# Kernel optimization log

Hardware: AMD Instinct MI355X
Metric: run time of the kernel (lower is better)

## Reference

```python
import jax, jax.numpy as jnp
import numpy as np

NTOKENS = 8192
TOPK = 2
E = 8
K = 1024  # hidden
N = 1024  # ffn shard (ffn_hidden // ffn_tp)


def setup_inputs() -> dict:
    key = jax.random.key(0)
    k1, k2, k3 = jax.random.split(key, 3)
    x = jax.random.normal(k1, (NTOKENS, K), jnp.float32) * 0.02
    # weights stored [E, N, K] (transpose_weight=True path in the torch module)
    weights = jax.random.normal(k2, (E, N, K), jnp.float32) * 0.02
    # random top-k expert assignment per token, then derive the expert-sorted
    # dispatch permutation (scatter_index) and per-expert counts (splits),
    # exactly the invariants flux.prepare_moe_ag_scatter_args relies on.
    experts = jax.random.randint(k3, (NTOKENS, TOPK), 0, E)
    flat = experts.reshape(-1)                       # [NTOKENS*TOPK]
    order = jnp.argsort(flat, stable=True)           # output row -> flat slot
    m = NTOKENS * TOPK
    pos = jnp.zeros((m,), jnp.int32).at[order].set(jnp.arange(m, dtype=jnp.int32))
    scatter_index = pos.reshape(NTOKENS, TOPK)       # flat slot -> output row
    splits = jnp.bincount(flat, length=E).astype(jnp.int32)
    return {"x": x, "weights": weights, "scatter_index": scatter_index, "splits": splits}


def reference(x, weights, scatter_index, splits):
    """MoE AG-scatter grouped GEMM (single-rank semantics: all-gather = identity).

    For each output row s (rows sorted by expert): out[s] = x[token(s)] @ W[e(s)].T
    where token(s) = gather_A_index[s] // topk and e(s) comes from splits.
    """
    ntokens, topk = scatter_index.shape
    e, n, k = weights.shape
    m_out = ntokens * topk  # total dispatched rows
    # inverse permutation: output row s -> flattened (token, slot) index
    gather_a = jnp.argsort(scatter_index.reshape(-1), stable=True)  # [m_out]
    token_of_row = gather_a // topk                                  # [m_out]
    expert_of_row = jnp.repeat(jnp.arange(e, dtype=jnp.int32), splits,
                               total_repeat_length=m_out)            # [m_out]
    # compute each token against every expert once (E/topk redundancy), then
    # gather the (token, expert) pairs -- avoids per-row weight materialization
    y_all = jnp.einsum('tk,enk->ten', x, weights)   # [ntokens, E, N]
    out = y_all[token_of_row, expert_of_row]        # [m_out, N]
    return out
```

## Files before the change

### kernel.cpp

```cpp
#include <hip/hip_runtime.h>
#include <hip/hip_bf16.h>

#define NTOK   8192
#define TOPK   2
#define NEXP   8
#define KDIM   1024
#define NDIM   1024
#define MOUT   (NTOK * TOPK)
#define BM     128
#define BN     128
#define BK     64
#define MAXT   (MOUT / BM + NEXP)
#define NBLK   (MAXT * (NDIM / BN))
#define CLSCAP (NBLK / 8)

#define ROWTOK   16384
#define XB_OFF   (128 * 1024)
#define XB_BYTES (NTOK * KDIM * 2)
#define WB_OFF   (XB_OFF + XB_BYTES)
#define WB_BYTES (NEXP * NDIM * KDIM * 2)
#define WS_NEED  ((size_t)(WB_OFF + WB_BYTES))

typedef unsigned short ushort_t;
typedef __attribute__((ext_vector_type(8))) short short8;
typedef __attribute__((ext_vector_type(4))) float floatx4;
typedef __attribute__((address_space(1))) const unsigned int gu32;
typedef __attribute__((address_space(3))) unsigned int lu32;

__device__ __forceinline__ void map_block(int b, const int* __restrict__ splits,
                                          int& row0, int& rows, int& e_out,
                                          int& cy) {
  int sp[8], off[8], n[8], take[8];
  int o = 0;
#pragma unroll
  for (int e = 0; e < 8; ++e) {
    sp[e] = splits[e];
    off[e] = o;
    o += sp[e];
    int tiles = (sp[e] + BM - 1) / BM;
    n[e] = 8 * tiles;
    take[e] = (n[e] < CLSCAP) ? n[e] : CLSCAP;
  }
  const int c = b & 7, i = b >> 3;
  int e = -1, j = 0;
  if (i < take[c]) {
    e = c; j = i;
  } else {
    int freeBefore = 0;
#pragma unroll
    for (int cc = 0; cc < 8; ++cc)
      if (cc < c) freeBefore += CLSCAP - take[cc];
    int spos = freeBefore + (i - take[c]);
    int acc = 0;
#pragma unroll
    for (int ee = 0; ee < 8; ++ee) {
      int sp_e = n[ee] - take[ee];
      if (e < 0 && spos < acc + sp_e) { e = ee; j = CLSCAP + (spos - acc); }
      acc += sp_e;
    }
    if (e < 0) { rows = 0; return; }
  }
  int t = j >> 3;
  cy = j & 7;
  row0 = off[e] + t * BM;
  int rem = off[e] + sp[e] - row0;
  rows = (rem > BM) ? BM : rem;
  if (rows < 0) rows = 0;
  e_out = e;
}

__global__ __launch_bounds__(256)
void convert_setup(const float* __restrict__ x, const float* __restrict__ w,
                   const int* __restrict__ scatter,
                   ushort_t* __restrict__ xb, ushort_t* __restrict__ wb,
                   int* __restrict__ ws) {
  const int N4X = NTOK * KDIM / 4;
  const int N4W = NEXP * NDIM * KDIM / 4;
  int gtid = blockIdx.x * 256 + threadIdx.x;

  if (gtid < MOUT) {
    int s = scatter[gtid];
    ws[ROWTOK + s] = gtid / TOPK;
  }

  for (int i = gtid; i < N4X + N4W; i += gridDim.x * 256) {
    float4 v = (i < N4X) ? ((const float4*)x)[i] : ((const float4*)w)[i - N4X];
    union { __hip_bfloat162 h; unsigned int u; } lo, hi;
    lo.h = __float22bfloat162_rn(make_float2(v.x, v.y));
    hi.h = __float22bfloat162_rn(make_float2(v.z, v.w));
    uint2 u2; u2.x = lo.u; u2.y = hi.u;
    if (i < N4X) ((uint2*)xb)[i] = u2;
    else         ((uint2*)wb)[i - N4X] = u2;
  }
}

__global__ __launch_bounds__(256, 3)
void moe_gemm_fast(const ushort_t* __restrict__ xb,
                   const ushort_t* __restrict__ wbm,
                   const int* __restrict__ splits,
                   const int* __restrict__ ws,
                   float* __restrict__ out) {
  __shared__ ushort_t As[BM * BK];
  __shared__ ushort_t Bs[BN * BK];

  int row0, rows, e, cyi;
  map_block(blockIdx.x, splits, row0, rows, e, cyi);
  if (rows == 0) return;
  const int c0 = cyi * BN;

  const int tid  = threadIdx.x;
  const int lane = tid & 63;
  const int wave = tid >> 6;
  const int wm   = (wave >> 1) * 64;
  const int wn   = (wave & 1) * 64;
  const int quad = lane >> 4;
  const int l16  = lane & 15;

  const int* __restrict__ row_token = ws + ROWTOK;

  const int lrow8  = lane >> 3;
  const int gchunk = (lane & 7) ^ lrow8;

  const ushort_t* aptr[4];
  const ushort_t* bptr[4];
#pragma unroll
  for (int t = 0; t < 4; ++t) {
    int r  = wave * 32 + t * 8 + lrow8;
    int rc = (r < rows) ? r : (rows - 1);
    aptr[t] = xb + (size_t)row_token[row0 + rc] * KDIM + gchunk * 8;
    bptr[t] = wbm + ((size_t)e * NDIM + c0 + r) * KDIM + gchunk * 8;
  }

  floatx4 zero = {0.f, 0.f, 0.f, 0.f};
  floatx4 acc[4][4];
#pragma unroll
  for (int i = 0; i < 4; ++i)
#pragma unroll
    for (int j = 0; j < 4; ++j) acc[i][j] = zero;

#pragma unroll 4
  for (int kk = 0; kk < KDIM; kk += BK) {
#pragma unroll
    for (int t = 0; t < 4; ++t) {
      __builtin_amdgcn_global_load_lds(
          (gu32*)(const void*)(aptr[t] + kk),
          (lu32*)(void*)(As + (wave * 32 + t * 8) * BK), 16, 0, 0);
      __builtin_amdgcn_global_load_lds(
          (gu32*)(const void*)(bptr[t] + kk),
          (lu32*)(void*)(Bs + (wave * 32 + t * 8) * BK), 16, 0, 0);
    }
    __syncthreads();

#pragma unroll
    for (int k2 = 0; k2 < 2; ++k2) {
      short8 af[4], bf[4];
#pragma unroll
      for (int i = 0; i < 4; ++i) {
        int m = wm + i * 16 + l16;
        af[i] = *(const short8*)(&As[m * BK + (((k2 * 4 + quad) ^ (m & 7)) * 8)]);
      }
#pragma unroll
      for (int j = 0; j < 4; ++j) {
        int n = wn + j * 16 + l16;
        bf[j] = *(const short8*)(&Bs[n * BK + (((k2 * 4 + quad) ^ (n & 7)) * 8)]);
      }
#pragma unroll
      for (int i = 0; i < 4; ++i)
#pragma unroll
        for (int j = 0; j < 4; ++j)
          acc[i][j] = __builtin_amdgcn_mfma_f32_16x16x32_bf16(af[i], bf[j],
                                                              acc[i][j], 0, 0, 0);
    }
    __syncthreads();
  }

#pragma unroll
  for (int i = 0; i < 4; ++i) {
#pragma unroll
    for (int r = 0; r < 4; ++r) {
      int lrow = wm + i * 16 + quad * 4 + r;
      if (lrow < rows) {
        float* o = out + (size_t)(row0 + lrow) * NDIM + c0 + wn + l16;
#pragma unroll
        for (int j = 0; j < 4; ++j) o[j * 16] = acc[i][j][r];
      }
    }
  }
}

__global__ void setup_only(const int* __restrict__ scatter,
                           int* __restrict__ ws) {
  int gtid = blockIdx.x * blockDim.x + threadIdx.x;
  if (gtid < MOUT) {
    int s = scatter[gtid];
    ws[ROWTOK + s] = gtid / TOPK;
  }
}

__global__ __launch_bounds__(256)
void moe_gemm_fallback(const float* __restrict__ x,
                       const float* __restrict__ w,
                       const int* __restrict__ splits,
                       const int* __restrict__ ws,
                       float* __restrict__ out) {
  __shared__ ushort_t As[BM * BK];
  __shared__ ushort_t Bs[BN * BK];

  int row0, rows, e, cyi;
  map_block(blockIdx.x, splits, row0, rows, e, cyi);
  if (rows == 0) return;
  const int c0 = cyi * BN;

  const int tid  = threadIdx.x;
  const int lane = tid & 63;
  const int wave = tid >> 6;
  const int wm   = (wave >> 1) * 64;
  const int wn   = (wave & 1) * 64;
  const int quad = lane >> 4;
  const int l16  = lane & 15;

  const int* __restrict__ row_token = ws + ROWTOK;

  const int f4    = tid & 15;
  const int rbase = tid >> 4;
  const int swz   = (f4 >> 1) ^ (rbase & 7);
  const int wroff = rbase * BK + swz * 8 + (f4 & 1) * 4;

  const float* __restrict__ wb = w + ((size_t)e * NDIM + c0) * KDIM;
  const float* pA[8];
#pragma unroll
  for (int i = 0; i < 8; ++i) {
    int r = rbase + i * 16;
    pA[i] = (r < rows) ? (x + (size_t)row_token[row0 + r] * KDIM + f4 * 4)
                       : nullptr;
  }
  const float* pB0 = wb + (size_t)rbase * KDIM + f4 * 4;

  floatx4 zero = {0.f, 0.f, 0.f, 0.f};
  floatx4 acc[4][4];
#pragma unroll
  for (int i = 0; i < 4; ++i)
#pragma unroll
    for (int j = 0; j < 4; ++j) acc[i][j] = zero;

#pragma unroll 1
  for (int kk = 0; kk < KDIM; kk += BK) {
#pragma unroll
    for (int i = 0; i < 8; ++i) {
      float4 v = {0.f, 0.f, 0.f, 0.f};
      if (pA[i]) v = *(const float4*)(pA[i] + kk);
      union { __hip_bfloat162 h; unsigned int u; } lo, hi;
      lo.h = __float22bfloat162_rn(make_float2(v.x, v.y));
      hi.h = __float22bfloat162_rn(make_float2(v.z, v.w));
      uint2 u2; u2.x = lo.u; u2.y = hi.u;
      *(uint2*)(&As[wroff + i * 16 * BK]) = u2;
    }
#pragma unroll
    for (int i = 0; i < 8; ++i) {
      float4 v = *(const float4*)(pB0 + (size_t)i * 16 * KDIM + kk);
      union { __hip_bfloat162 h; unsigned int u; } lo, hi;
      lo.h = __float22bfloat162_rn(make_float2(v.x, v.y));
      hi.h = __float22bfloat162_rn(make_float2(v.z, v.w));
      uint2 u2; u2.x = lo.u; u2.y = hi.u;
      *(uint2*)(&Bs[wroff + i * 16 * BK]) = u2;
    }
    __syncthreads();
#pragma unroll
    for (int k2 = 0; k2 < 2; ++k2) {
      short8 af[4], bf[4];
#pragma unroll
      for (int i = 0; i < 4; ++i) {
        int m = wm + i * 16 + l16;
        af[i] = *(const short8*)(&As[m * BK + ((k2 * 4 + quad) ^ (m & 7)) * 8]);
      }
#pragma unroll
      for (int j = 0; j < 4; ++j) {
        int n = wn + j * 16 + l16;
        bf[j] = *(const short8*)(&Bs[n * BK + ((k2 * 4 + quad) ^ (n & 7)) * 8]);
      }
#pragma unroll
      for (int i = 0; i < 4; ++i)
#pragma unroll
        for (int j = 0; j < 4; ++j)
          acc[i][j] = __builtin_amdgcn_mfma_f32_16x16x32_bf16(af[i], bf[j],
                                                              acc[i][j], 0, 0, 0);
    }
    __syncthreads();
  }

#pragma unroll
  for (int i = 0; i < 4; ++i) {
#pragma unroll
    for (int r = 0; r < 4; ++r) {
      int lrow = wm + i * 16 + quad * 4 + r;
      if (lrow < rows) {
        float* o = out + (size_t)(row0 + lrow) * NDIM + c0 + wn + l16;
#pragma unroll
        for (int j = 0; j < 4; ++j) o[j * 16] = acc[i][j][r];
      }
    }
  }
}

extern "C" void kernel_launch(void* const* d_in, const int* in_sizes, int n_in,
                              void* d_out, int out_size, void* d_ws, size_t ws_size,
                              hipStream_t stream) {
  const float* x       = (const float*)d_in[0];
  const float* weights = (const float*)d_in[1];
  const int*   scatter = (const int*)d_in[2];
  const int*   splits  = (const int*)d_in[3];
  float*       out     = (float*)d_out;
  int*         ws      = (int*)d_ws;

  if (ws_size >= WS_NEED) {
    ushort_t* xb = (ushort_t*)((char*)d_ws + XB_OFF);
    ushort_t* wb = (ushort_t*)((char*)d_ws + WB_OFF);
    convert_setup<<<dim3(2048), dim3(256), 0, stream>>>(x, weights, scatter,
                                                        xb, wb, ws);
    moe_gemm_fast<<<dim3(NBLK), dim3(256), 0, stream>>>(xb, wb, splits, ws, out);
  } else {
    setup_only<<<dim3(MOUT / 256), dim3(256), 0, stream>>>(scatter, ws);
    moe_gemm_fallback<<<dim3(NBLK), dim3(256), 0, stream>>>(x, weights, splits,
                                                            ws, out);
  }
}
```

Baseline: 156.1 us.

## Fuse activation fp32-to-bf16 conversion into GEMM A-tile loads

The separate pre-pass that converted x to bf16 is removed. The GEMM now loads fp32 activation rows directly into registers, converts them to bf16 and writes the swizzled A tile to LDS, while B still uses async global_load_lds. The weight conversion kernel is widened to process 8 floats per thread with 16-byte stores. This drops one full read/write pass over x, but each gathered row is now read in fp32 (twice the bytes) by every column tile that uses it, and the A path becomes synchronous through registers.

```diff
diff --git a/kernel.cpp b/kernel.cpp
--- a/kernel.cpp
+++ b/kernel.cpp
@@ -15,9 +15,7 @@
 #define CLSCAP (NBLK / 8)
 
 #define ROWTOK   16384
-#define XB_OFF   (128 * 1024)
-#define XB_BYTES (NTOK * KDIM * 2)
-#define WB_OFF   (XB_OFF + XB_BYTES)
+#define WB_OFF   (128 * 1024)
 #define WB_BYTES (NEXP * NDIM * KDIM * 2)
 #define WS_NEED  ((size_t)(WB_OFF + WB_BYTES))
 
@@ -70,12 +68,9 @@
 }
 
 __global__ __launch_bounds__(256)
-void convert_setup(const float* __restrict__ x, const float* __restrict__ w,
-                   const int* __restrict__ scatter,
-                   ushort_t* __restrict__ xb, ushort_t* __restrict__ wb,
-                   int* __restrict__ ws) {
-  const int N4X = NTOK * KDIM / 4;
-  const int N4W = NEXP * NDIM * KDIM / 4;
+void convert_w(const float* __restrict__ w, const int* __restrict__ scatter,
+               ushort_t* __restrict__ wb, int* __restrict__ ws) {
+  const int N8W = NEXP * NDIM * KDIM / 8;
   int gtid = blockIdx.x * 256 + threadIdx.x;
 
   if (gtid < MOUT) {
@@ -83,19 +78,22 @@
     ws[ROWTOK + s] = gtid / TOPK;
   }
 
-  for (int i = gtid; i < N4X + N4W; i += gridDim.x * 256) {
-    float4 v = (i < N4X) ? ((const float4*)x)[i] : ((const float4*)w)[i - N4X];
-    union { __hip_bfloat162 h; unsigned int u; } lo, hi;
-    lo.h = __float22bfloat162_rn(make_float2(v.x, v.y));
-    hi.h = __float22bfloat162_rn(make_float2(v.z, v.w));
-    uint2 u2; u2.x = lo.u; u2.y = hi.u;
-    if (i < N4X) ((uint2*)xb)[i] = u2;
-    else         ((uint2*)wb)[i - N4X] = u2;
+  for (int i = gtid; i < N8W; i += gridDim.x * 256) {
+    const float4* src = ((const float4*)w) + 2 * (size_t)i;
+    float4 v0 = src[0];
+    float4 v1 = src[1];
+    union { __hip_bfloat162 h; unsigned int u; } p0, p1, p2, p3;
+    p0.h = __float22bfloat162_rn(make_float2(v0.x, v0.y));
+    p1.h = __float22bfloat162_rn(make_float2(v0.z, v0.w));
+    p2.h = __float22bfloat162_rn(make_float2(v1.x, v1.y));
+    p3.h = __float22bfloat162_rn(make_float2(v1.z, v1.w));
+    uint4 u4; u4.x = p0.u; u4.y = p1.u; u4.z = p2.u; u4.w = p3.u;
+    ((uint4*)wb)[i] = u4;
   }
 }
 
 __global__ __launch_bounds__(256, 3)
-void moe_gemm_fast(const ushort_t* __restrict__ xb,
+void moe_gemm_fast(const float* __restrict__ x,
                    const ushort_t* __restrict__ wbm,
                    const int* __restrict__ splits,
                    const int* __restrict__ ws,
@@ -119,15 +117,22 @@
   const int* __restrict__ row_token = ws + ROWTOK;
 
   const int lrow8  = lane >> 3;
-  const int gchunk = (lane & 7) ^ lrow8;
-
-  const ushort_t* aptr[4];
-  const ushort_t* bptr[4];
+  const int chunk  = lane & 7;
+  const int gchunk = chunk ^ lrow8;
+
+  const float* ax[4];
 #pragma unroll
   for (int t = 0; t < 4; ++t) {
     int r  = wave * 32 + t * 8 + lrow8;
     int rc = (r < rows) ? r : (rows - 1);
-    aptr[t] = xb + (size_t)row_token[row0 + rc] * KDIM + gchunk * 8;
+    ax[t] = x + (size_t)row_token[row0 + rc] * KDIM + chunk * 8;
+  }
+  const int awofs = (wave * 32 + lrow8) * BK + ((chunk ^ lrow8) * 8);
+
+  const ushort_t* bptr[4];
+#pragma unroll
+  for (int t = 0; t < 4; ++t) {
+    int r = wave * 32 + t * 8 + lrow8;
     bptr[t] = wbm + ((size_t)e * NDIM + c0 + r) * KDIM + gchunk * 8;
   }
 
@@ -138,16 +143,29 @@
 #pragma unroll
     for (int j = 0; j < 4; ++j) acc[i][j] = zero;
 
-#pragma unroll 4
+#pragma unroll 2
   for (int kk = 0; kk < KDIM; kk += BK) {
 #pragma unroll
     for (int t = 0; t < 4; ++t) {
-      __builtin_amdgcn_global_load_lds(
-          (gu32*)(const void*)(aptr[t] + kk),
-          (lu32*)(void*)(As + (wave * 32 + t * 8) * BK), 16, 0, 0);
       __builtin_amdgcn_global_load_lds(
           (gu32*)(const void*)(bptr[t] + kk),
           (lu32*)(void*)(Bs + (wave * 32 + t * 8) * BK), 16, 0, 0);
+    }
+    float4 va[4][2];
+#pragma unroll
+    for (int t = 0; t < 4; ++t) {
+      va[t][0] = *(const float4*)(ax[t] + kk);
+      va[t][1] = *(const float4*)(ax[t] + kk + 4);
+    }
+#pragma unroll
+    for (int t = 0; t < 4; ++t) {
+      union { __hip_bfloat162 h; unsigned int u; } p0, p1, p2, p3;
+      p0.h = __float22bfloat162_rn(make_float2(va[t][0].x, va[t][0].y));
+      p1.h = __float22bfloat162_rn(make_float2(va[t][0].z, va[t][0].w));
+      p2.h = __float22bfloat162_rn(make_float2(va[t][1].x, va[t][1].y));
+      p3.h = __float22bfloat162_rn(make_float2(va[t][1].z, va[t][1].w));
+      uint4 u4; u4.x = p0.u; u4.y = p1.u; u4.z = p2.u; u4.w = p3.u;
+      *(uint4*)(&As[awofs + t * 8 * BK]) = u4;
     }
     __syncthreads();
 
@@ -313,11 +331,9 @@
   int*         ws      = (int*)d_ws;
 
   if (ws_size >= WS_NEED) {
-    ushort_t* xb = (ushort_t*)((char*)d_ws + XB_OFF);
     ushort_t* wb = (ushort_t*)((char*)d_ws + WB_OFF);
-    convert_setup<<<dim3(2048), dim3(256), 0, stream>>>(x, weights, scatter,
-                                                        xb, wb, ws);
-    moe_gemm_fast<<<dim3(NBLK), dim3(256), 0, stream>>>(xb, wb, splits, ws, out);
+    convert_w<<<dim3(2048), dim3(256), 0, stream>>>(weights, scatter, wb, ws);
+    moe_gemm_fast<<<dim3(NBLK), dim3(256), 0, stream>>>(x, wb, splits, ws, out);
   } else {
     setup_only<<<dim3(MOUT / 256), dim3(256), 0, stream>>>(scatter, ws);
     moe_gemm_fallback<<<dim3(NBLK), dim3(256), 0, stream>>>(x, weights, splits,
```

Measured after the change: 178.3 us. 14.2% more time.
